# Performance work log

Hardware: AMD Instinct MI355X
Metric: run time of the kernel (lower is better)

## Reference

```python
import jax, jax.numpy as jnp
import numpy as np

B, S, HID = 2, 2048, 2048
H, KV, D = 16, 8, 128          # query heads, kv heads, head_dim
EPS = 1e-6
THETA = 1000000.0


def setup_inputs() -> dict:
    key = jax.random.key(0)
    ks = jax.random.split(key, 8)
    sc = 0.02
    hidden_states = jax.random.normal(ks[0], (B, S, HID), dtype=jnp.float32)
    Wq = jax.random.normal(ks[1], (HID, H * D), dtype=jnp.float32) * sc
    Wk = jax.random.normal(ks[2], (HID, KV * D), dtype=jnp.float32) * sc
    Wv = jax.random.normal(ks[3], (HID, KV * D), dtype=jnp.float32) * sc
    Wo = jax.random.normal(ks[4], (H * D, HID), dtype=jnp.float32) * sc
    q_norm_w = jnp.ones((D,), dtype=jnp.float32)
    k_norm_w = jnp.ones((D,), dtype=jnp.float32)
    positions = jnp.arange(S, dtype=jnp.int32)
    # causal mask: True = masked (j > i)
    attention_mask = jnp.triu(jnp.ones((S, S), dtype=bool), k=1)
    return {
        "hidden_states": hidden_states, "Wq": Wq, "Wk": Wk, "Wv": Wv,
        "Wo": Wo, "q_norm_w": q_norm_w, "k_norm_w": k_norm_w,
        "positions": positions, "attention_mask": attention_mask,
    }


def _rms_norm(x, w):
    # x: [..., D]; RMSNorm over last dim
    var = jnp.mean(x * x, axis=-1, keepdims=True)
    return x * jax.lax.rsqrt(var + EPS) * w


def _rope(x, positions):
    # x: [B, h, S, D]; standard rotate-half RoPE
    inv_freq = 1.0 / (THETA ** (jnp.arange(0, D, 2, dtype=jnp.float32) / D))
    ang = positions.astype(jnp.float32)[:, None] * inv_freq[None, :]  # [S, D/2]
    cos = jnp.concatenate([jnp.cos(ang), jnp.cos(ang)], axis=-1)      # [S, D]
    sin = jnp.concatenate([jnp.sin(ang), jnp.sin(ang)], axis=-1)
    x1, x2 = x[..., : D // 2], x[..., D // 2:]
    rot = jnp.concatenate([-x2, x1], axis=-1)
    return x * cos + rot * sin


def reference(hidden_states, Wq, Wk, Wv, Wo, q_norm_w, k_norm_w,
              positions, attention_mask):
    b, s, _ = hidden_states.shape
    q = (hidden_states @ Wq).reshape(b, s, H, D).transpose(0, 2, 1, 3)   # [B,H,S,D]
    k = (hidden_states @ Wk).reshape(b, s, KV, D).transpose(0, 2, 1, 3)  # [B,KV,S,D]
    v = (hidden_states @ Wv).reshape(b, s, KV, D).transpose(0, 2, 1, 3)
    q = _rms_norm(q, q_norm_w)
    k = _rms_norm(k, k_norm_w)
    q = _rope(q, positions)
    k = _rope(k, positions)
    # GQA: repeat kv heads
    g = H // KV
    k = jnp.repeat(k, g, axis=1)  # [B,H,S,D]
    v = jnp.repeat(v, g, axis=1)
    scale = 1.0 / np.sqrt(D).astype(np.float32)
    scores = jnp.einsum('bhqd,bhkd->bhqk', q, k) * scale
    scores = jnp.where(attention_mask[None, None, :, :], -jnp.inf, scores)
    attn = jax.nn.softmax(scores, axis=-1)
    out = jnp.einsum('bhqk,bhkd->bhqd', attn, v)
    out = out.transpose(0, 2, 1, 3).reshape(b, s, H * D)
    return out @ Wo
```

## Files before the change

kernel.cpp:

```cpp
#include <hip/hip_runtime.h>
#include <hip/hip_bf16.h>

typedef __hip_bfloat16 bf16;
typedef __attribute__((ext_vector_type(8))) short short8v;
typedef __attribute__((ext_vector_type(4))) float f32x4;

constexpr int nB = 2;
constexpr int nS = 2048;
constexpr int nHID = 2048;
constexpr int nH = 16;
constexpr int nKV = 8;
constexpr int nD = 128;
constexpr int QS = 4096;
constexpr float kEps = 1e-6f;
constexpr float kScale = 0.08838834764831845f;

template <int N>
struct IC {
  static constexpr int value = N;
};

__device__ inline float b2f(unsigned short u) {
  return __uint_as_float(((unsigned)u) << 16);
}
__device__ inline float bf2f(bf16 v) { return __bfloat162float(v); }
__device__ inline short f2bs(float f) {
  bf16 h = __float2bfloat16(f);
  return *reinterpret_cast<short*>(&h);
}
__device__ inline unsigned pack2bf(float a, float b) {
  return ((unsigned)(unsigned short)f2bs(b) << 16) |
         (unsigned)(unsigned short)f2bs(a);
}

__device__ inline void gload_lds16(const bf16* g, bf16* l) {
  __builtin_amdgcn_global_load_lds(
      (const __attribute__((address_space(1))) void*)g,
      (__attribute__((address_space(3))) void*)l, 16, 0, 0);
}

template <int N>
__device__ inline void vwait() {
  asm volatile("s_waitcnt vmcnt(%0)" ::"n"(N) : "memory");
}

__global__ __launch_bounds__(256) void cvt_f32_bf16(
    const float* __restrict__ src, bf16* __restrict__ dst, int n) {
  const int i = (blockIdx.x * 256 + threadIdx.x) * 4;
  if (i >= n) return;
  const float4 v = *reinterpret_cast<const float4*>(src + i);
  ushort4 o;
  o.x = (unsigned short)f2bs(v.x);
  o.y = (unsigned short)f2bs(v.y);
  o.z = (unsigned short)f2bs(v.z);
  o.w = (unsigned short)f2bs(v.w);
  *reinterpret_cast<ushort4*>(dst + i) = o;
}

__global__ __launch_bounds__(256) void transpose_f32_bf16(
    const float* __restrict__ src, bf16* __restrict__ dst, int K, int N) {
  __shared__ float t[32][33];
  const int k0 = blockIdx.y * 32, n0 = blockIdx.x * 32;
  const int c = threadIdx.x & 31, r8 = threadIdx.x >> 5;
#pragma unroll
  for (int i = 0; i < 4; ++i)
    t[r8 + i * 8][c] = src[(size_t)(k0 + r8 + i * 8) * N + n0 + c];
  __syncthreads();
#pragma unroll
  for (int i = 0; i < 4; ++i)
    dst[(size_t)(n0 + r8 + i * 8) * K + k0 + c] =
        __float2bfloat16(t[c][r8 + i * 8]);
}

template <int BM, typename OUT_T>
__global__ __launch_bounds__(512) void gemm_8ph(
    const bf16* __restrict__ A, const bf16* __restrict__ Bt,
    OUT_T* __restrict__ C, int M, int N, int K) {
  constexpr int LA = BM / 128;
  constexpr int LB = 2;
  constexpr int MF = BM / 32;
  constexpr int MFH = MF / 2;
  constexpr int W = 2 * (LA + LB);
  constexpr int LDSB = 2 * BM * 32 + 2 * 256 * 32;
  __shared__ bf16 lds[2 * LDSB];

  const int tid = threadIdx.x;
  const int wave = tid >> 6, lane = tid & 63;
  const int lr = lane & 15, lg = lane >> 4;
  const int wm = wave >> 2, wn = wave & 3;
  const int m0 = blockIdx.y * BM, n0 = blockIdx.x * 256;
  const int srow = tid >> 2, scol = (tid & 3) * 8;

  auto stageA = [&](int t, int kk) {
    bf16* dst = lds + (t & 1) * LDSB + kk * (BM * 32) + wave * 512;
    const bf16* src = A + (size_t)(m0 + srow) * K + t * 64 + kk * 32 + scol;
#pragma unroll
    for (int j = 0; j < LA; ++j)
      gload_lds16(src + (size_t)(j * 128) * K, dst + j * 4096);
  };
  auto stageB = [&](int t, int kk) {
    bf16* dst =
        lds + (t & 1) * LDSB + 2 * BM * 32 + kk * (256 * 32) + wave * 512;
    const bf16* src = Bt + (size_t)(n0 + srow) * K + t * 64 + kk * 32 + scol;
#pragma unroll
    for (int j = 0; j < LB; ++j)
      gload_lds16(src + (size_t)(j * 128) * K, dst + j * 4096);
  };

  f32x4 acc[MF][4];
#pragma unroll
  for (int m = 0; m < MF; ++m)
#pragma unroll
    for (int n = 0; n < 4; ++n) acc[m][n] = (f32x4){0.f, 0.f, 0.f, 0.f};
  short8v bfr[4];

  auto phase = [&](auto WC, int buf, int kk, int mh, auto stageFn) {
    constexpr int WAIT = decltype(WC)::value;
    if constexpr (WAIT >= 0) vwait<WAIT>();
    __builtin_amdgcn_s_barrier();
    asm volatile("" ::: "memory");
    if (mh == 0) {
      const bf16* bb = lds + buf * LDSB + 2 * BM * 32 + kk * (256 * 32);
#pragma unroll
      for (int ni = 0; ni < 4; ++ni)
        bfr[ni] = *reinterpret_cast<const short8v*>(
            bb + (wn * 64 + ni * 16 + lr) * 32 + lg * 8);
    }
    short8v af[MFH];
    const bf16* ab = lds + buf * LDSB + kk * (BM * 32);
#pragma unroll
    for (int ii = 0; ii < MFH; ++ii)
      af[ii] = *reinterpret_cast<const short8v*>(
          ab + (wm * (BM / 2) + (mh * MFH + ii) * 16 + lr) * 32 + lg * 8);
    stageFn();
    asm volatile("s_waitcnt lgkmcnt(0)" ::: "memory");
    __builtin_amdgcn_sched_barrier(0);
    __builtin_amdgcn_s_setprio(1);
#pragma unroll
    for (int ii = 0; ii < MFH; ++ii)
#pragma unroll
      for (int ni = 0; ni < 4; ++ni)
        acc[mh * MFH + ii][ni] = __builtin_amdgcn_mfma_f32_16x16x32_bf16(
            af[ii], bfr[ni], acc[mh * MFH + ii][ni], 0, 0, 0);
    __builtin_amdgcn_s_setprio(0);
  };

  const int NT = K / 64;
  stageA(0, 0);
  stageB(0, 0);
  stageA(0, 1);
  stageB(0, 1);
  stageA(1, 0);
  stageB(1, 0);

  for (int t = 0; t < NT - 1; ++t) {
    const int buf = t & 1;
    phase(IC<W>{}, buf, 0, 0, [&] { stageA(t + 1, 1); });
    phase(IC<-1>{}, buf, 0, 1, [&] { stageB(t + 1, 1); });
    phase(IC<W>{}, buf, 1, 0, [&] {
      if (t < NT - 2) stageA(t + 2, 0);
    });
    phase(IC<-1>{}, buf, 1, 1, [&] {
      if (t < NT - 2) stageB(t + 2, 0);
    });
  }
  {
    const int buf = (NT - 1) & 1;
    phase(IC<LA + LB>{}, buf, 0, 0, [&] {});
    phase(IC<-1>{}, buf, 0, 1, [&] {});
    phase(IC<0>{}, buf, 1, 0, [&] {});
    phase(IC<-1>{}, buf, 1, 1, [&] {});
  }

#pragma unroll
  for (int m = 0; m < MF; ++m)
#pragma unroll
    for (int n = 0; n < 4; ++n)
#pragma unroll
      for (int r = 0; r < 4; ++r) {
        const int row = m0 + wm * (BM / 2) + m * 16 + 4 * lg + r;
        const int col = n0 + wn * 64 + n * 16 + lr;
        if constexpr (sizeof(OUT_T) == 2)
          C[(size_t)row * N + col] = __float2bfloat16(acc[m][n][r]);
        else
          C[(size_t)row * N + col] = acc[m][n][r];
      }
}

__global__ __launch_bounds__(128) void norm_rope_fused(
    bf16* __restrict__ qkv, const float* __restrict__ qw,
    const float* __restrict__ kw) {
  const int row = blockIdx.x;
  const int head = blockIdx.y;
  const int t = threadIdx.x;
  const int s = row & (nS - 1);
  const bool isQ = head < nH;
  const int col = isQ ? head * nD : 2048 + (head - nH) * nD;
  const float* w = isQ ? qw : kw;
  bf16* xp = qkv + (size_t)row * QS + col;
  const float v = bf2f(xp[t]);
  float ss = v * v;
#pragma unroll
  for (int off = 32; off > 0; off >>= 1) ss += __shfl_xor(ss, off);
  __shared__ float wsum[2];
  __shared__ float buf[nD];
  if ((t & 63) == 0) wsum[t >> 6] = ss;
  __syncthreads();
  const float inv = rsqrtf((wsum[0] + wsum[1]) * (1.0f / nD) + kEps);
  const float nv = v * inv * w[t];
  buf[t] = nv;
  __syncthreads();
  const float partner = buf[t ^ 64];
  const float rot = (t < 64) ? -partner : partner;
  const int j = t & 63;
  const float invf = expf(-(float)j * (13.815510557964274f / 64.0f));
  const float ang = (float)s * invf;
  const float outv = nv * cosf(ang) + rot * sinf(ang);
  xp[t] = __float2bfloat16(outv);
}

constexpr int BQ = 64, BKT = 64;

__global__ __launch_bounds__(256) void attn_mfma(
    const bf16* __restrict__ QKV, bf16* __restrict__ O) {
  const int pair = blockIdx.x;
  const int bh = blockIdx.y;
  const int b = bh >> 4, h = bh & 15, kvh = h >> 1;
  const int tid = threadIdx.x;
  const int wave = tid >> 6, lane = tid & 63;
  const int lr = lane & 15, lg = lane >> 4;

  __shared__ bf16 Ks[BKT][136];
  __shared__ bf16 Vt[nD][72];
  __shared__ bf16 Pl[4][16][72];

  const bf16* Qbase = QKV + (size_t)b * nS * QS + h * nD;
  const bf16* Kbase = QKV + (size_t)b * nS * QS + 2048 + kvh * nD;
  const bf16* Vbase = QKV + (size_t)b * nS * QS + 3072 + kvh * nD;

  const int krow = tid >> 2, kcc = (tid & 3) * 32;
  const int vkey = tid & 63, vdc = (tid >> 6) * 32;

  short8v kreg[4], vreg[4];
  auto gload = [&](int kt) {
    const bf16* ksrc = Kbase + (size_t)(kt + krow) * QS + kcc;
    const bf16* vsrc = Vbase + (size_t)(kt + vkey) * QS + vdc;
#pragma unroll
    for (int i = 0; i < 4; ++i) {
      kreg[i] = *reinterpret_cast<const short8v*>(ksrc + 8 * i);
      vreg[i] = *reinterpret_cast<const short8v*>(vsrc + 8 * i);
    }
  };
  auto lwrite = [&]() {
#pragma unroll
    for (int i = 0; i < 4; ++i)
      *reinterpret_cast<short8v*>(&Ks[krow][kcc + 8 * i]) = kreg[i];
#pragma unroll
    for (int i = 0; i < 4; ++i)
#pragma unroll
      for (int j = 0; j < 8; ++j)
        *reinterpret_cast<short*>(&Vt[vdc + 8 * i + j][vkey]) = vreg[i][j];
  };

  short8v qf[4];
  f32x4 of[8];
  float m_run, l_run;

  auto load_q = [&](int q0) {
    const bf16* qrow = Qbase + (size_t)(q0 + 16 * wave + lr) * QS;
#pragma unroll
    for (int dc = 0; dc < 4; ++dc)
      qf[dc] = *reinterpret_cast<const short8v*>(qrow + 32 * dc + 8 * lg);
  };

  auto run_tiles = [&](int q0, int nt, bool stage_next0) {
    m_run = -1e30f;
    l_run = 0.f;
#pragma unroll
    for (int n = 0; n < 8; ++n) of[n] = (f32x4){0.f, 0.f, 0.f, 0.f};
    for (int j = 0; j < nt; ++j) {
      const int kt = j * BKT;
      const bool have_next = (j + 1 < nt) || stage_next0;
      const int ktn = (j + 1 < nt) ? (j + 1) * BKT : 0;
      if (have_next) gload(ktn);

      f32x4 s[4];
      __builtin_amdgcn_s_setprio(1);
#pragma unroll
      for (int sub = 0; sub < 4; ++sub) {
        f32x4 acc = {0.f, 0.f, 0.f, 0.f};
#pragma unroll
        for (int dc = 0; dc < 4; ++dc) {
          const short8v kf = *reinterpret_cast<const short8v*>(
              &Ks[16 * sub + lr][32 * dc + 8 * lg]);
          acc = __builtin_amdgcn_mfma_f32_16x16x32_bf16(kf, qf[dc], acc, 0, 0,
                                                        0);
        }
        s[sub] = acc;
      }
      __builtin_amdgcn_s_setprio(0);

      const bool diag = (kt == q0);
#pragma unroll
      for (int sub = 0; sub < 4; ++sub)
#pragma unroll
        for (int r = 0; r < 4; ++r) {
          float v = s[sub][r] * kScale;
          if (diag && (16 * sub + 4 * lg + r > 16 * wave + lr)) v = -1e30f;
          s[sub][r] = v;
        }

      float pmax = -1e30f;
#pragma unroll
      for (int sub = 0; sub < 4; ++sub)
#pragma unroll
        for (int r = 0; r < 4; ++r) pmax = fmaxf(pmax, s[sub][r]);
      pmax = fmaxf(pmax, __shfl_xor(pmax, 16));
      pmax = fmaxf(pmax, __shfl_xor(pmax, 32));

      if (!__all(pmax - m_run <= 8.f)) {
        const float mt = fmaxf(m_run, pmax);
        const float corr = __expf(m_run - mt);
#pragma unroll
        for (int n = 0; n < 8; ++n) of[n] *= corr;
        l_run *= corr;
        m_run = mt;
      }

      float p[4][4];
      float lsum = 0.f;
#pragma unroll
      for (int sub = 0; sub < 4; ++sub)
#pragma unroll
        for (int r = 0; r < 4; ++r) {
          const float e = __expf(s[sub][r] - m_run);
          p[sub][r] = e;
          lsum += e;
        }
      lsum += __shfl_xor(lsum, 16);
      lsum += __shfl_xor(lsum, 32);
      l_run += lsum;

#pragma unroll
      for (int sub = 0; sub < 4; ++sub)
#pragma unroll
        for (int rp = 0; rp < 2; ++rp)
          *reinterpret_cast<unsigned*>(
              &Pl[wave][lr][16 * sub + 4 * lg + 2 * rp]) =
              pack2bf(p[sub][2 * rp], p[sub][2 * rp + 1]);

      __builtin_amdgcn_s_setprio(1);
#pragma unroll
      for (int kk = 0; kk < 2; ++kk) {
        const short8v pb = *reinterpret_cast<const short8v*>(
            &Pl[wave][lr][32 * kk + 8 * lg]);
#pragma unroll
        for (int n = 0; n < 8; ++n) {
          const short8v vf = *reinterpret_cast<const short8v*>(
              &Vt[16 * n + lr][32 * kk + 8 * lg]);
          of[n] =
              __builtin_amdgcn_mfma_f32_16x16x32_bf16(vf, pb, of[n], 0, 0, 0);
        }
      }
      __builtin_amdgcn_s_setprio(0);

      if (have_next) {
        __syncthreads();
        lwrite();
        __syncthreads();
      }
    }
  };

  auto epilogue = [&](int q0) {
    const float inv = 1.0f / l_run;
    bf16* orow = O + ((size_t)(b * nS + q0 + 16 * wave + lr)) * (nH * nD) +
                 h * nD + 4 * lg;
#pragma unroll
    for (int n = 0; n < 8; ++n)
#pragma unroll
      for (int rp = 0; rp < 2; ++rp)
        *reinterpret_cast<unsigned*>(orow + 16 * n + 2 * rp) =
            pack2bf(of[n][2 * rp] * inv, of[n][2 * rp + 1] * inv);
  };

  const int qh = (31 - pair) * BQ, nth = 32 - pair;
  const int ql = pair * BQ, ntl = pair + 1;

  gload(0);
  lwrite();
  __syncthreads();

  load_q(qh);
  run_tiles(qh, nth, true);
  epilogue(qh);

  load_q(ql);
  run_tiles(ql, ntl, false);
  epilogue(ql);
}

extern "C" void kernel_launch(void* const* d_in, const int* in_sizes, int n_in,
                              void* d_out, int out_size, void* d_ws,
                              size_t ws_size, hipStream_t stream) {
  const float* hs = (const float*)d_in[0];
  const float* Wq = (const float*)d_in[1];
  const float* Wk = (const float*)d_in[2];
  const float* Wv = (const float*)d_in[3];
  const float* Wo = (const float*)d_in[4];
  const float* qw = (const float*)d_in[5];
  const float* kw = (const float*)d_in[6];

  const int M = nB * nS;
  char* ws = (char*)d_ws;
  size_t off = 0;
  auto alloc = [&](size_t bytes) {
    char* p = ws + off;
    off += bytes;
    return p;
  };
  bf16* hsb = (bf16*)alloc((size_t)M * nHID * 2);
  bf16* att = hsb;
  bf16* qkv = (bf16*)alloc((size_t)M * QS * 2);
  bf16* Wcat = (bf16*)alloc((size_t)QS * nHID * 2);
  bf16* Wot = (bf16*)alloc((size_t)nH * nD * nHID * 2);
  float* out = (float*)d_out;

  const int nHsElems = M * nHID;
  cvt_f32_bf16<<<(nHsElems / 4 + 255) / 256, 256, 0, stream>>>(hs, hsb,
                                                               nHsElems);
  transpose_f32_bf16<<<dim3(nH * nD / 32, nHID / 32), 256, 0, stream>>>(
      Wq, Wcat, nHID, nH * nD);
  transpose_f32_bf16<<<dim3(nKV * nD / 32, nHID / 32), 256, 0, stream>>>(
      Wk, Wcat + (size_t)2048 * nHID, nHID, nKV * nD);
  transpose_f32_bf16<<<dim3(nKV * nD / 32, nHID / 32), 256, 0, stream>>>(
      Wv, Wcat + (size_t)3072 * nHID, nHID, nKV * nD);
  transpose_f32_bf16<<<dim3(nHID / 32, nH * nD / 32), 256, 0, stream>>>(
      Wo, Wot, nH * nD, nHID);

  gemm_8ph<256, bf16><<<dim3(QS / 256, M / 256), 512, 0, stream>>>(
      hsb, Wcat, qkv, M, QS, nHID);

  norm_rope_fused<<<dim3(M, nH + nKV), 128, 0, stream>>>(qkv, qw, kw);

  attn_mfma<<<dim3(16, nB * nH), 256, 0, stream>>>(qkv, att);

  gemm_8ph<128, float><<<dim3(nHID / 256, M / 128), 512, 0, stream>>>(
      att, Wot, out, M, nHID, nH * nD);
}
```

Before: 262.0 us.

## Restructure attention to 128-row query blocks and move GEMM barriers

The attention kernel drops the paired short/long query-tile scheme. Each 512-thread block now handles one 128-row query block with eight waves sharing the K/V tiles in shared memory, and blocks are launched in a 1D grid ordered so the longest causal blocks start first. The aim is more K/V reuse per staged tile and better load balance. Separately, the GEMM phase loop moves its workgroup barrier to after the LDS reads and adds one after the MFMAs, with a prologue wait, changing how the pipelined loads are synchronised. Per-wave masking now checks whether each wave's rows intersect the diagonal.

New measurement: 266.2 us. Within noise of the previous version (+1.6%).

```diff
diff --git a/kernel.cpp b/kernel.cpp
--- a/kernel.cpp
+++ b/kernel.cpp
@@ -78,9 +78,9 @@
     OUT_T* __restrict__ C, int M, int N, int K) {
   constexpr int LA = BM / 128;
   constexpr int LB = 2;
+  constexpr int H = LA + LB;
   constexpr int MF = BM / 32;
   constexpr int MFH = MF / 2;
-  constexpr int W = 2 * (LA + LB);
   constexpr int LDSB = 2 * BM * 32 + 2 * 256 * 32;
   __shared__ bf16 lds[2 * LDSB];
 
@@ -117,8 +117,6 @@
   auto phase = [&](auto WC, int buf, int kk, int mh, auto stageFn) {
     constexpr int WAIT = decltype(WC)::value;
     if constexpr (WAIT >= 0) vwait<WAIT>();
-    __builtin_amdgcn_s_barrier();
-    asm volatile("" ::: "memory");
     if (mh == 0) {
       const bf16* bb = lds + buf * LDSB + 2 * BM * 32 + kk * (256 * 32);
 #pragma unroll
@@ -133,6 +131,8 @@
       af[ii] = *reinterpret_cast<const short8v*>(
           ab + (wm * (BM / 2) + (mh * MFH + ii) * 16 + lr) * 32 + lg * 8);
     stageFn();
+    __builtin_amdgcn_sched_barrier(0);
+    __builtin_amdgcn_s_barrier();
     asm volatile("s_waitcnt lgkmcnt(0)" ::: "memory");
     __builtin_amdgcn_sched_barrier(0);
     __builtin_amdgcn_s_setprio(1);
@@ -143,6 +143,7 @@
         acc[mh * MFH + ii][ni] = __builtin_amdgcn_mfma_f32_16x16x32_bf16(
             af[ii], bfr[ni], acc[mh * MFH + ii][ni], 0, 0, 0);
     __builtin_amdgcn_s_setprio(0);
+    __builtin_amdgcn_s_barrier();
   };
 
   const int NT = K / 64;
@@ -152,12 +153,14 @@
   stageB(0, 1);
   stageA(1, 0);
   stageB(1, 0);
+  vwait<2 * H>();
+  __builtin_amdgcn_s_barrier();
 
   for (int t = 0; t < NT - 1; ++t) {
     const int buf = t & 1;
-    phase(IC<W>{}, buf, 0, 0, [&] { stageA(t + 1, 1); });
+    phase(IC<H>{}, buf, 0, 0, [&] { stageA(t + 1, 1); });
     phase(IC<-1>{}, buf, 0, 1, [&] { stageB(t + 1, 1); });
-    phase(IC<W>{}, buf, 1, 0, [&] {
+    phase(IC<H>{}, buf, 1, 0, [&] {
       if (t < NT - 2) stageA(t + 2, 0);
     });
     phase(IC<-1>{}, buf, 1, 1, [&] {
@@ -166,9 +169,9 @@
   }
   {
     const int buf = (NT - 1) & 1;
-    phase(IC<LA + LB>{}, buf, 0, 0, [&] {});
+    phase(IC<0>{}, buf, 0, 0, [&] {});
     phase(IC<-1>{}, buf, 0, 1, [&] {});
-    phase(IC<0>{}, buf, 1, 0, [&] {});
+    phase(IC<-1>{}, buf, 1, 0, [&] {});
     phase(IC<-1>{}, buf, 1, 1, [&] {});
   }
 
@@ -219,160 +222,160 @@
   xp[t] = __float2bfloat16(outv);
 }
 
-constexpr int BQ = 64, BKT = 64;
-
-__global__ __launch_bounds__(256) void attn_mfma(
+constexpr int BQ = 128, BKT = 64;
+
+__global__ __launch_bounds__(512) void attn_mfma(
     const bf16* __restrict__ QKV, bf16* __restrict__ O) {
-  const int pair = blockIdx.x;
-  const int bh = blockIdx.y;
+  const int l = blockIdx.x;
+  const int bh = l & 31;
+  const int rr0 = l >> 5;
+  const int qb = (rr0 < 8) ? 15 - rr0 : rr0 - 8;
   const int b = bh >> 4, h = bh & 15, kvh = h >> 1;
+  const int q0 = qb * BQ;
+  const int nt = 2 * qb + 2;
   const int tid = threadIdx.x;
   const int wave = tid >> 6, lane = tid & 63;
   const int lr = lane & 15, lg = lane >> 4;
 
   __shared__ bf16 Ks[BKT][136];
   __shared__ bf16 Vt[nD][72];
-  __shared__ bf16 Pl[4][16][72];
+  __shared__ bf16 Pl[8][16][72];
 
   const bf16* Qbase = QKV + (size_t)b * nS * QS + h * nD;
   const bf16* Kbase = QKV + (size_t)b * nS * QS + 2048 + kvh * nD;
   const bf16* Vbase = QKV + (size_t)b * nS * QS + 3072 + kvh * nD;
 
-  const int krow = tid >> 2, kcc = (tid & 3) * 32;
-  const int vkey = tid & 63, vdc = (tid >> 6) * 32;
-
-  short8v kreg[4], vreg[4];
+  const int krow = tid >> 3, kcc = (tid & 7) * 16;
+  const int vkey = tid & 63, vdc = (tid >> 6) * 16;
+
+  short8v kreg[2], vreg[2];
   auto gload = [&](int kt) {
     const bf16* ksrc = Kbase + (size_t)(kt + krow) * QS + kcc;
     const bf16* vsrc = Vbase + (size_t)(kt + vkey) * QS + vdc;
-#pragma unroll
-    for (int i = 0; i < 4; ++i) {
-      kreg[i] = *reinterpret_cast<const short8v*>(ksrc + 8 * i);
-      vreg[i] = *reinterpret_cast<const short8v*>(vsrc + 8 * i);
-    }
+    kreg[0] = *reinterpret_cast<const short8v*>(ksrc);
+    kreg[1] = *reinterpret_cast<const short8v*>(ksrc + 8);
+    vreg[0] = *reinterpret_cast<const short8v*>(vsrc);
+    vreg[1] = *reinterpret_cast<const short8v*>(vsrc + 8);
   };
   auto lwrite = [&]() {
-#pragma unroll
-    for (int i = 0; i < 4; ++i)
-      *reinterpret_cast<short8v*>(&Ks[krow][kcc + 8 * i]) = kreg[i];
-#pragma unroll
-    for (int i = 0; i < 4; ++i)
+    *reinterpret_cast<short8v*>(&Ks[krow][kcc]) = kreg[0];
+    *reinterpret_cast<short8v*>(&Ks[krow][kcc + 8]) = kreg[1];
+#pragma unroll
+    for (int i = 0; i < 2; ++i)
 #pragma unroll
       for (int j = 0; j < 8; ++j)
         *reinterpret_cast<short*>(&Vt[vdc + 8 * i + j][vkey]) = vreg[i][j];
   };
 
   short8v qf[4];
-  f32x4 of[8];
-  float m_run, l_run;
-
-  auto load_q = [&](int q0) {
+  {
     const bf16* qrow = Qbase + (size_t)(q0 + 16 * wave + lr) * QS;
 #pragma unroll
     for (int dc = 0; dc < 4; ++dc)
       qf[dc] = *reinterpret_cast<const short8v*>(qrow + 32 * dc + 8 * lg);
-  };
-
-  auto run_tiles = [&](int q0, int nt, bool stage_next0) {
-    m_run = -1e30f;
-    l_run = 0.f;
-#pragma unroll
-    for (int n = 0; n < 8; ++n) of[n] = (f32x4){0.f, 0.f, 0.f, 0.f};
-    for (int j = 0; j < nt; ++j) {
-      const int kt = j * BKT;
-      const bool have_next = (j + 1 < nt) || stage_next0;
-      const int ktn = (j + 1 < nt) ? (j + 1) * BKT : 0;
-      if (have_next) gload(ktn);
-
-      f32x4 s[4];
-      __builtin_amdgcn_s_setprio(1);
-#pragma unroll
-      for (int sub = 0; sub < 4; ++sub) {
-        f32x4 acc = {0.f, 0.f, 0.f, 0.f};
-#pragma unroll
-        for (int dc = 0; dc < 4; ++dc) {
-          const short8v kf = *reinterpret_cast<const short8v*>(
-              &Ks[16 * sub + lr][32 * dc + 8 * lg]);
-          acc = __builtin_amdgcn_mfma_f32_16x16x32_bf16(kf, qf[dc], acc, 0, 0,
-                                                        0);
-        }
-        s[sub] = acc;
+  }
+
+  f32x4 of[8];
+#pragma unroll
+  for (int n = 0; n < 8; ++n) of[n] = (f32x4){0.f, 0.f, 0.f, 0.f};
+  float m_run = -1e30f, l_run = 0.f;
+
+  gload(0);
+  lwrite();
+  __syncthreads();
+
+  for (int j = 0; j < nt; ++j) {
+    const int kt = j * BKT;
+    const bool have_next = (j + 1 < nt);
+    if (have_next) gload((j + 1) * BKT);
+
+    f32x4 s[4];
+    __builtin_amdgcn_s_setprio(1);
+#pragma unroll
+    for (int sub = 0; sub < 4; ++sub) {
+      f32x4 acc = {0.f, 0.f, 0.f, 0.f};
+#pragma unroll
+      for (int dc = 0; dc < 4; ++dc) {
+        const short8v kf = *reinterpret_cast<const short8v*>(
+            &Ks[16 * sub + lr][32 * dc + 8 * lg]);
+        acc = __builtin_amdgcn_mfma_f32_16x16x32_bf16(kf, qf[dc], acc, 0, 0, 0);
       }
-      __builtin_amdgcn_s_setprio(0);
-
-      const bool diag = (kt == q0);
-#pragma unroll
-      for (int sub = 0; sub < 4; ++sub)
-#pragma unroll
-        for (int r = 0; r < 4; ++r) {
-          float v = s[sub][r] * kScale;
-          if (diag && (16 * sub + 4 * lg + r > 16 * wave + lr)) v = -1e30f;
-          s[sub][r] = v;
-        }
-
-      float pmax = -1e30f;
-#pragma unroll
-      for (int sub = 0; sub < 4; ++sub)
-#pragma unroll
-        for (int r = 0; r < 4; ++r) pmax = fmaxf(pmax, s[sub][r]);
-      pmax = fmaxf(pmax, __shfl_xor(pmax, 16));
-      pmax = fmaxf(pmax, __shfl_xor(pmax, 32));
-
-      if (!__all(pmax - m_run <= 8.f)) {
-        const float mt = fmaxf(m_run, pmax);
-        const float corr = __expf(m_run - mt);
-#pragma unroll
-        for (int n = 0; n < 8; ++n) of[n] *= corr;
-        l_run *= corr;
-        m_run = mt;
+      s[sub] = acc;
+    }
+    __builtin_amdgcn_s_setprio(0);
+
+    const bool needMask = (kt + BKT > q0 + 16 * wave);
+#pragma unroll
+    for (int sub = 0; sub < 4; ++sub)
+#pragma unroll
+      for (int r = 0; r < 4; ++r) {
+        float v = s[sub][r] * kScale;
+        if (needMask && (kt + 16 * sub + 4 * lg + r > q0 + 16 * wave + lr))
+          v = -1e30f;
+        s[sub][r] = v;
       }
 
-      float p[4][4];
-      float lsum = 0.f;
-#pragma unroll
-      for (int sub = 0; sub < 4; ++sub)
-#pragma unroll
-        for (int r = 0; r < 4; ++r) {
-          const float e = __expf(s[sub][r] - m_run);
-          p[sub][r] = e;
-          lsum += e;
-        }
-      lsum += __shfl_xor(lsum, 16);
-      lsum += __shfl_xor(lsum, 32);
-      l_run += lsum;
-
-#pragma unroll
-      for (int sub = 0; sub < 4; ++sub)
-#pragma unroll
-        for (int rp = 0; rp < 2; ++rp)
-          *reinterpret_cast<unsigned*>(
-              &Pl[wave][lr][16 * sub + 4 * lg + 2 * rp]) =
-              pack2bf(p[sub][2 * rp], p[sub][2 * rp + 1]);
-
-      __builtin_amdgcn_s_setprio(1);
-#pragma unroll
-      for (int kk = 0; kk < 2; ++kk) {
-        const short8v pb = *reinterpret_cast<const short8v*>(
-            &Pl[wave][lr][32 * kk + 8 * lg]);
-#pragma unroll
-        for (int n = 0; n < 8; ++n) {
-          const short8v vf = *reinterpret_cast<const short8v*>(
-              &Vt[16 * n + lr][32 * kk + 8 * lg]);
-          of[n] =
-              __builtin_amdgcn_mfma_f32_16x16x32_bf16(vf, pb, of[n], 0, 0, 0);
-        }
+    float pmax = -1e30f;
+#pragma unroll
+    for (int sub = 0; sub < 4; ++sub)
+#pragma unroll
+      for (int r = 0; r < 4; ++r) pmax = fmaxf(pmax, s[sub][r]);
+    pmax = fmaxf(pmax, __shfl_xor(pmax, 16));
+    pmax = fmaxf(pmax, __shfl_xor(pmax, 32));
+
+    if (!__all(pmax - m_run <= 8.f)) {
+      const float mt = fmaxf(m_run, pmax);
+      const float corr = __expf(m_run - mt);
+#pragma unroll
+      for (int n = 0; n < 8; ++n) of[n] *= corr;
+      l_run *= corr;
+      m_run = mt;
+    }
+
+    float p[4][4];
+    float lsum = 0.f;
+#pragma unroll
+    for (int sub = 0; sub < 4; ++sub)
+#pragma unroll
+      for (int r = 0; r < 4; ++r) {
+        const float e = __expf(s[sub][r] - m_run);
+        p[sub][r] = e;
+        lsum += e;
       }
-      __builtin_amdgcn_s_setprio(0);
-
-      if (have_next) {
-        __syncthreads();
-        lwrite();
-        __syncthreads();
+    lsum += __shfl_xor(lsum, 16);
+    lsum += __shfl_xor(lsum, 32);
+    l_run += lsum;
+
+#pragma unroll
+    for (int sub = 0; sub < 4; ++sub)
+#pragma unroll
+      for (int rp = 0; rp < 2; ++rp)
+        *reinterpret_cast<unsigned*>(
+            &Pl[wave][lr][16 * sub + 4 * lg + 2 * rp]) =
+            pack2bf(p[sub][2 * rp], p[sub][2 * rp + 1]);
+
+    __builtin_amdgcn_s_setprio(1);
+#pragma unroll
+    for (int kk = 0; kk < 2; ++kk) {
+      const short8v pb =
+          *reinterpret_cast<const short8v*>(&Pl[wave][lr][32 * kk + 8 * lg]);
+#pragma unroll
+      for (int n = 0; n < 8; ++n) {
+        const short8v vf = *reinterpret_cast<const short8v*>(
+            &Vt[16 * n + lr][32 * kk + 8 * lg]);
+        of[n] = __builtin_amdgcn_mfma_f32_16x16x32_bf16(vf, pb, of[n], 0, 0, 0);
       }
     }
-  };
-
-  auto epilogue = [&](int q0) {
+    __builtin_amdgcn_s_setprio(0);
+
+    if (have_next) {
+      __syncthreads();
+      lwrite();
+      __syncthreads();
+    }
+  }
+
+  {
     const float inv = 1.0f / l_run;
     bf16* orow = O + ((size_t)(b * nS + q0 + 16 * wave + lr)) * (nH * nD) +
                  h * nD + 4 * lg;
@@ -382,22 +385,7 @@
       for (int rp = 0; rp < 2; ++rp)
         *reinterpret_cast<unsigned*>(orow + 16 * n + 2 * rp) =
             pack2bf(of[n][2 * rp] * inv, of[n][2 * rp + 1] * inv);
-  };
-
-  const int qh = (31 - pair) * BQ, nth = 32 - pair;
-  const int ql = pair * BQ, ntl = pair + 1;
-
-  gload(0);
-  lwrite();
-  __syncthreads();
-
-  load_q(qh);
-  run_tiles(qh, nth, true);
-  epilogue(qh);
-
-  load_q(ql);
-  run_tiles(ql, ntl, false);
-  epilogue(ql);
+  }
 }
 
 extern "C" void kernel_launch(void* const* d_in, const int* in_sizes, int n_in,
@@ -443,7 +431,7 @@
 
   norm_rope_fused<<<dim3(M, nH + nKV), 128, 0, stream>>>(qkv, qw, kw);
 
-  attn_mfma<<<dim3(16, nB * nH), 256, 0, stream>>>(qkv, att);
+  attn_mfma<<<dim3(512), 512, 0, stream>>>(qkv, att);
 
   gemm_8ph<128, float><<<dim3(nHID / 256, M / 128), 512, 0, stream>>>(
       att, Wot, out, M, nHID, nH * nD);
```
